# Kernel tuning notes

Measured on AMD Instinct MI355X. Metric: run time of the kernel, lower is better.

## Reference

```python
import jax, jax.numpy as jnp
import numpy as np

B, N, DIM, H, K = 2, 8192, 256, 8, 32
HD = DIM // H


def setup_inputs() -> dict:
    key = jax.random.key(0)
    ks = jax.random.split(key, 10)
    s = 1.0 / np.sqrt(DIM)
    return {
        "x": jax.random.normal(ks[0], (B, N, DIM), jnp.float32),
        "xyz": jax.random.normal(ks[1], (B, N, 3), jnp.float32),
        "idx": jax.random.randint(ks[2], (B, N, K), 0, N, jnp.int32),
        "Wq": jax.random.normal(ks[3], (DIM, DIM), jnp.float32) * s,
        "bq": jnp.zeros((DIM,), jnp.float32),
        "Wk": jax.random.normal(ks[4], (DIM, DIM), jnp.float32) * s,
        "bk": jnp.zeros((DIM,), jnp.float32),
        "Wv": jax.random.normal(ks[5], (DIM, DIM), jnp.float32) * s,
        "bv": jnp.zeros((DIM,), jnp.float32),
        "Wo": jax.random.normal(ks[6], (DIM, DIM), jnp.float32) * s,
        "bo": jnp.zeros((DIM,), jnp.float32),
        "W1": jax.random.normal(ks[7], (3, 32), jnp.float32) * 0.5,
        "b1": jnp.zeros((32,), jnp.float32),
        "W2": jax.random.normal(ks[8], (32, H), jnp.float32) * 0.2,
        "b2": jnp.zeros((H,), jnp.float32),
    }


def reference(x, xyz, idx, Wq, bq, Wk, bk, Wv, bv, Wo, bo, W1, b1, W2, b2):
    Bn, Nn, C = x.shape
    k = idx.shape[-1]
    q = (x @ Wq + bq).reshape(Bn, Nn, H, HD)          # [B,N,H,hd]
    kf = (x @ Wk + bk).reshape(Bn, Nn, H, HD)
    vf = (x @ Wv + bv).reshape(Bn, Nn, H, HD)
    # gather k neighbors per point (per-batch fancy indexing)
    gather = jax.vmap(lambda f, i: f[i])               # [N,H,hd],[N,k] -> [N,k,H,hd]
    kn = gather(kf, idx)                               # [B,N,k,H,hd]
    vn = gather(vf, idx)
    nxyz = jax.vmap(lambda p, i: p[i])(xyz, idx)       # [B,N,k,3]
    rel = xyz[:, :, None, :] - nxyz                    # [B,N,k,3]
    bias = jax.nn.relu(rel @ W1 + b1) @ W2 + b2        # [B,N,k,H]
    scores = jnp.einsum('bnhd,bnkhd->bnhk', q, kn) / np.sqrt(HD).astype(np.float32)
    scores = scores + bias.transpose(0, 1, 3, 2)       # [B,N,H,k]
    attn = jax.nn.softmax(scores, axis=-1)
    out = jnp.einsum('bnhk,bnkhd->bnhd', attn, vn).reshape(Bn, Nn, C)
    return out @ Wo + bo
```

## Files before the change

### kernel.cpp

```cpp
#include <hip/hip_runtime.h>
#include <hip/hip_bf16.h>

typedef unsigned int uint32;
typedef unsigned short ushort;
typedef __attribute__((ext_vector_type(4))) float floatx4;
typedef __attribute__((ext_vector_type(8))) __bf16 bf16x8;

#define NPTS 8192

__device__ __forceinline__ ushort f2bf(float f) {
    uint32 u = __float_as_uint(f);
    uint32 r = (u + 0x7fffu + ((u >> 16) & 1u)) >> 16;
    return (ushort)r;
}
__device__ __forceinline__ float bf1(ushort u) { return __uint_as_float((uint32)u << 16); }
__device__ __forceinline__ float bflo(uint32 u) { return __uint_as_float(u << 16); }
__device__ __forceinline__ float bfhi(uint32 u) { return __uint_as_float(u & 0xffff0000u); }

__global__ __launch_bounds__(256) void prep_kernel(
    const float* __restrict__ x, const float* __restrict__ xyz, const int* __restrict__ idx,
    const float* __restrict__ Wq, const float* __restrict__ Wk,
    const float* __restrict__ Wv, const float* __restrict__ Wo,
    const float* __restrict__ bq, const float* __restrict__ bk, const float* __restrict__ bv,
    const float* __restrict__ W1, const float* __restrict__ b1,
    const float* __restrict__ W2, const float* __restrict__ b2,
    ushort* __restrict__ xb, ushort* __restrict__ Wqkvt, ushort* __restrict__ Wot,
    float* __restrict__ biasqkv, ushort* __restrict__ bias_g) {
    const int bi = blockIdx.x;
    const int tid = threadIdx.x;
    if (bi < 4096) {
        int i = (bi * 256 + tid) * 4;
        float4 v = *(const float4*)(x + i);
        ushort4 o;
        o.x = f2bf(v.x); o.y = f2bf(v.y); o.z = f2bf(v.z); o.w = f2bf(v.w);
        *(ushort4*)(xb + i) = o;
    } else if (bi < 5120) {
        int f = (bi - 4096) * 256 + tid;
        if (f < 768 * 256) {
            int n = f >> 8, k = f & 255;
            int seg = n >> 8, nc = n & 255;
            const float* W = (seg == 0) ? Wq : (seg == 1) ? Wk : Wv;
            Wqkvt[f] = f2bf(W[k * 256 + nc]);
        } else {
            int g = f - 768 * 256;
            int n = g >> 8, k = g & 255;
            Wot[g] = f2bf(Wo[k * 256 + n]);
        }
        if (f < 768) biasqkv[f] = (f < 256) ? bq[f] : (f < 512) ? bk[f - 256] : bv[f - 512];
    } else {
        __shared__ float W1s[96], b1s[32], W2s[256], b2s[8];
        if (tid < 96) W1s[tid] = W1[tid];
        if (tid < 32) b1s[tid] = b1[tid];
        W2s[tid] = W2[tid];
        if (tid < 8) b2s[tid] = b2[tid];
        __syncthreads();
        const int wid = tid >> 6, lane = tid & 63;
        const int s = lane >> 5, j = lane & 31;
        const int p = (bi - 5120) * 8 + wid * 2 + s;
        const int b = p >> 13, n = p & 8191;
        const int nj = idx[(size_t)p * 32 + j];
        const size_t pb = ((size_t)b * NPTS + n) * 3;
        const size_t nb = ((size_t)b * NPTS + nj) * 3;
        const float rx = xyz[pb + 0] - xyz[nb + 0];
        const float ry = xyz[pb + 1] - xyz[nb + 1];
        const float rz = xyz[pb + 2] - xyz[nb + 2];
        float acc[8];
#pragma unroll
        for (int h = 0; h < 8; ++h) acc[h] = b2s[h];
#pragma unroll
        for (int u = 0; u < 32; ++u) {
            float hv = rx * W1s[u] + ry * W1s[32 + u] + rz * W1s[64 + u] + b1s[u];
            hv = fmaxf(hv, 0.f);
#pragma unroll
            for (int h = 0; h < 8; ++h) acc[h] += hv * W2s[u * 8 + h];
        }
#pragma unroll
        for (int h = 0; h < 8; ++h) bias_g[((size_t)p * 8 + h) * 32 + j] = f2bf(acc[h]);
    }
}

template <bool OUT_BF16>
__global__ __launch_bounds__(256) void gemm_mfma64(const ushort* __restrict__ A,
                                                   const ushort* __restrict__ Wt,
                                                   const float* __restrict__ bias,
                                                   void* __restrict__ outv, int N) {
    __shared__ __align__(16) ushort As[64 * 32];
    __shared__ __align__(16) ushort Bs[64 * 32];
    const int tid = threadIdx.x;
    const int w = tid >> 6, lane = tid & 63;
    const int m0 = blockIdx.y * 64, n0 = blockIdx.x * 64;

    const int row = tid >> 2;
    const int col16 = (tid & 3) * 16;

    floatx4 acc[4] = {};

    for (int kt = 0; kt < 256; kt += 32) {
        __syncthreads();
        {
            const char* ga = (const char*)(A + (size_t)(m0 + row) * 256 + kt) + col16;
            const char* gb = (const char*)(Wt + (size_t)(n0 + row) * 256 + kt) + col16;
            __builtin_amdgcn_global_load_lds((const __attribute__((address_space(1))) void*)ga,
                                             (__attribute__((address_space(3))) void*)((char*)As + w * 1024),
                                             16, 0, 0);
            __builtin_amdgcn_global_load_lds((const __attribute__((address_space(1))) void*)gb,
                                             (__attribute__((address_space(3))) void*)((char*)Bs + w * 1024),
                                             16, 0, 0);
        }
        __syncthreads();

        bf16x8 af = *(const bf16x8*)&As[(w * 16 + (lane & 15)) * 32 + (lane >> 4) * 8];
        bf16x8 bg[4];
#pragma unroll
        for (int ni = 0; ni < 4; ++ni)
            bg[ni] = *(const bf16x8*)&Bs[(ni * 16 + (lane & 15)) * 32 + (lane >> 4) * 8];
#pragma unroll
        for (int ni = 0; ni < 4; ++ni)
            acc[ni] = __builtin_amdgcn_mfma_f32_16x16x32_bf16(af, bg[ni], acc[ni], 0, 0, 0);
    }

#pragma unroll
    for (int ni = 0; ni < 4; ++ni) {
        const int col = n0 + ni * 16 + (lane & 15);
        const float bv = bias[col];
        const int row0 = m0 + w * 16 + (lane >> 4) * 4;
#pragma unroll
        for (int r = 0; r < 4; ++r) {
            const float v = acc[ni][r] + bv;
            if (OUT_BF16)
                ((ushort*)outv)[(size_t)(row0 + r) * N + col] = f2bf(v);
            else
                ((float*)outv)[(size_t)(row0 + r) * N + col] = v;
        }
    }
}

__global__ __launch_bounds__(256) void attn_kernel(
    const ushort* __restrict__ qkv, const int* __restrict__ idx,
    const ushort* __restrict__ bias_g, ushort* __restrict__ out) {
    __shared__ __align__(16) float q_s[4][2][32];
    __shared__ float e_s[4][2][32];
    __shared__ uint32 off_s[4][2][32];
    __shared__ float ssum_s[4][2];

    const int tid = threadIdx.x, wid = tid >> 6, lane = tid & 63;
    const int h = blockIdx.x & 7;
    const int pg = blockIdx.x >> 3;
    const int pbase = pg * 8 + wid * 2;
    const char* base = (const char*)qkv;

    const int s = lane >> 5, j = lane & 31;
    const int p = pbase + s;
    const int b = p >> 13;

    off_s[wid][s][j] = (uint32)(idx[(size_t)p * 32 + j] + b * NPTS) * 1536u;
    q_s[wid][s][j] = bf1(qkv[(size_t)p * 768 + h * 32 + j]);
    __syncthreads();

    {
        const uint4* kp = (const uint4*)(base + off_s[wid][s][j] + 512 + h * 64);
        float d = 0.f;
#pragma unroll
        for (int c = 0; c < 4; ++c) {
            uint4 kv = kp[c];
            float4 qa = *(const float4*)&q_s[wid][s][c * 8];
            float4 qb = *(const float4*)&q_s[wid][s][c * 8 + 4];
            d += bflo(kv.x) * qa.x + bfhi(kv.x) * qa.y
               + bflo(kv.y) * qa.z + bfhi(kv.y) * qa.w
               + bflo(kv.z) * qb.x + bfhi(kv.z) * qb.y
               + bflo(kv.w) * qb.z + bfhi(kv.w) * qb.w;
        }
        const float sc = d * 0.17677669529663687f + bf1(bias_g[((size_t)p * 8 + h) * 32 + j]);
        const float e = __expf(sc);
        float ssum = e;
#pragma unroll
        for (int msk = 16; msk >= 1; msk >>= 1) ssum += __shfl_xor(ssum, msk, 64);
        e_s[wid][s][j] = e;
        if (j == 0) ssum_s[wid][s] = ssum;
    }
    __syncthreads();

    {
        const int s2 = lane >> 5, hj = (lane >> 4) & 1, d2 = lane & 15;
        const int p2 = pbase + s2;
        const float rinv = __builtin_amdgcn_rcpf(ssum_s[wid][s2]);
        float ax = 0.f, ay = 0.f;
#pragma unroll
        for (int jj = 0; jj < 16; ++jj) {
            const int j2 = hj * 16 + jj;
            const float wgt = e_s[wid][s2][j2];
            const uint32 v = *(const uint32*)(base + off_s[wid][s2][j2] + 1024 + h * 64 + d2 * 4);
            ax += wgt * bflo(v);
            ay += wgt * bfhi(v);
        }
        ax += __shfl_xor(ax, 16, 64);
        ay += __shfl_xor(ay, 16, 64);
        if (hj == 0) {
            const uint32 o = (uint32)f2bf(ax * rinv) | ((uint32)f2bf(ay * rinv) << 16);
            *(uint32*)(out + (size_t)p2 * 256 + h * 32 + d2 * 2) = o;
        }
    }
}

extern "C" void kernel_launch(void* const* d_in, const int* in_sizes, int n_in,
                              void* d_out, int out_size, void* d_ws, size_t ws_size,
                              hipStream_t stream) {
    const float* x   = (const float*)d_in[0];
    const float* xyz = (const float*)d_in[1];
    const int*   idx = (const int*)d_in[2];
    const float* Wq = (const float*)d_in[3];
    const float* bq = (const float*)d_in[4];
    const float* Wk = (const float*)d_in[5];
    const float* bk = (const float*)d_in[6];
    const float* Wv = (const float*)d_in[7];
    const float* bv = (const float*)d_in[8];
    const float* Wo = (const float*)d_in[9];
    const float* bo = (const float*)d_in[10];
    const float* W1 = (const float*)d_in[11];
    const float* b1 = (const float*)d_in[12];
    const float* W2 = (const float*)d_in[13];
    const float* b2 = (const float*)d_in[14];

    char* wsb = (char*)d_ws;
    ushort* x_bf    = (ushort*)wsb;
    ushort* aout_bf = x_bf;
    ushort* qkv_bf  = (ushort*)(wsb + 8388608);
    ushort* Wqkvt   = (ushort*)(wsb + 33554432);
    ushort* Wot     = (ushort*)(wsb + 33947648);
    float*  biasqkv = (float*)(wsb + 34078720);
    ushort* bias_g  = (ushort*)(wsb + 34081792);

    prep_kernel<<<7168, 256, 0, stream>>>(x, xyz, idx, Wq, Wk, Wv, Wo, bq, bk, bv,
                                          W1, b1, W2, b2, x_bf, Wqkvt, Wot, biasqkv, bias_g);

    gemm_mfma64<true><<<dim3(12, 256), 256, 0, stream>>>(x_bf, Wqkvt, biasqkv, qkv_bf, 768);

    attn_kernel<<<16384, 256, 0, stream>>>(qkv_bf, idx, bias_g, aout_bf);

    gemm_mfma64<false><<<dim3(4, 256), 256, 0, stream>>>(aout_bf, Wot, bo, d_out, 256);
}
```

Before: 198.7 us.

## Use 128x128 swizzled-LDS tiles for QKV GEMM and vectorize attention V gather

```diff
diff --git a/kernel.cpp b/kernel.cpp
--- a/kernel.cpp
+++ b/kernel.cpp
@@ -79,17 +79,81 @@
     }
 }
 
-template <bool OUT_BF16>
+__global__ __launch_bounds__(256) void gemm_qkv(const ushort* __restrict__ A,
+                                                const ushort* __restrict__ Wt,
+                                                const float* __restrict__ bias,
+                                                ushort* __restrict__ outp) {
+    __shared__ __align__(16) ushort As[128 * 64];
+    __shared__ __align__(16) ushort Bs[128 * 64];
+    const int tid = threadIdx.x;
+    const int w = tid >> 6, lane = tid & 63;
+    const int m0 = blockIdx.y * 128, n0 = blockIdx.x * 128;
+    const int wm = (w & 1) * 64, wn = (w >> 1) * 64;
+    const int N = 768;
+
+    floatx4 acc[4][4] = {};
+
+    for (int kt = 0; kt < 256; kt += 64) {
+        __syncthreads();
+#pragma unroll
+        for (int c4 = 0; c4 < 4; ++c4) {
+            const int c = w * 4 + c4;
+            const int r = c * 8 + (lane >> 3);
+            const int gseg = (lane & 7) ^ (r & 7);
+            const char* ga = (const char*)(A + (size_t)(m0 + r) * 256 + kt) + gseg * 16;
+            const char* gb = (const char*)(Wt + (size_t)(n0 + r) * 256 + kt) + gseg * 16;
+            __builtin_amdgcn_global_load_lds((const __attribute__((address_space(1))) void*)ga,
+                                             (__attribute__((address_space(3))) void*)((char*)As + c * 1024),
+                                             16, 0, 0);
+            __builtin_amdgcn_global_load_lds((const __attribute__((address_space(1))) void*)gb,
+                                             (__attribute__((address_space(3))) void*)((char*)Bs + c * 1024),
+                                             16, 0, 0);
+        }
+        __syncthreads();
+
+        bf16x8 af[2][4], bg[2][4];
+#pragma unroll
+        for (int kk = 0; kk < 2; ++kk) {
+            const int s = kk * 4 + (lane >> 4);
+            const int phys = s ^ (lane & 7);
+#pragma unroll
+            for (int i = 0; i < 4; ++i) {
+                af[kk][i] = *(const bf16x8*)((const char*)As + (wm + i * 16 + (lane & 15)) * 128 + phys * 16);
+                bg[kk][i] = *(const bf16x8*)((const char*)Bs + (wn + i * 16 + (lane & 15)) * 128 + phys * 16);
+            }
+        }
+#pragma unroll
+        for (int kk = 0; kk < 2; ++kk)
+#pragma unroll
+            for (int mi = 0; mi < 4; ++mi)
+#pragma unroll
+                for (int ni = 0; ni < 4; ++ni)
+                    acc[mi][ni] = __builtin_amdgcn_mfma_f32_16x16x32_bf16(af[kk][mi], bg[kk][ni], acc[mi][ni], 0, 0, 0);
+    }
+
+#pragma unroll
+    for (int ni = 0; ni < 4; ++ni) {
+        const int col = n0 + wn + ni * 16 + (lane & 15);
+        const float bv = bias[col];
+#pragma unroll
+        for (int mi = 0; mi < 4; ++mi) {
+            const int row0 = m0 + wm + mi * 16 + (lane >> 4) * 4;
+#pragma unroll
+            for (int r = 0; r < 4; ++r)
+                outp[(size_t)(row0 + r) * N + col] = f2bf(acc[mi][ni][r] + bv);
+        }
+    }
+}
+
 __global__ __launch_bounds__(256) void gemm_mfma64(const ushort* __restrict__ A,
                                                    const ushort* __restrict__ Wt,
                                                    const float* __restrict__ bias,
-                                                   void* __restrict__ outv, int N) {
+                                                   float* __restrict__ outv, int N) {
     __shared__ __align__(16) ushort As[64 * 32];
     __shared__ __align__(16) ushort Bs[64 * 32];
     const int tid = threadIdx.x;
     const int w = tid >> 6, lane = tid & 63;
     const int m0 = blockIdx.y * 64, n0 = blockIdx.x * 64;
-
     const int row = tid >> 2;
     const int col16 = (tid & 3) * 16;
 
@@ -125,13 +189,8 @@
         const float bv = bias[col];
         const int row0 = m0 + w * 16 + (lane >> 4) * 4;
 #pragma unroll
-        for (int r = 0; r < 4; ++r) {
-            const float v = acc[ni][r] + bv;
-            if (OUT_BF16)
-                ((ushort*)outv)[(size_t)(row0 + r) * N + col] = f2bf(v);
-            else
-                ((float*)outv)[(size_t)(row0 + r) * N + col] = v;
-        }
+        for (int r = 0; r < 4; ++r)
+            outv[(size_t)(row0 + r) * N + col] = acc[ni][r] + bv;
     }
 }
 
@@ -181,23 +240,34 @@
     __syncthreads();
 
     {
-        const int s2 = lane >> 5, hj = (lane >> 4) & 1, d2 = lane & 15;
+        const int s2 = lane >> 5;
+        const int q4 = (lane >> 3) & 3;
+        const int j3 = lane & 7;
         const int p2 = pbase + s2;
-        const float rinv = __builtin_amdgcn_rcpf(ssum_s[wid][s2]);
-        float ax = 0.f, ay = 0.f;
-#pragma unroll
-        for (int jj = 0; jj < 16; ++jj) {
-            const int j2 = hj * 16 + jj;
+        float a[8] = {};
+#pragma unroll
+        for (int t = 0; t < 4; ++t) {
+            const int j2 = t * 8 + j3;
             const float wgt = e_s[wid][s2][j2];
-            const uint32 v = *(const uint32*)(base + off_s[wid][s2][j2] + 1024 + h * 64 + d2 * 4);
-            ax += wgt * bflo(v);
-            ay += wgt * bfhi(v);
-        }
-        ax += __shfl_xor(ax, 16, 64);
-        ay += __shfl_xor(ay, 16, 64);
-        if (hj == 0) {
-            const uint32 o = (uint32)f2bf(ax * rinv) | ((uint32)f2bf(ay * rinv) << 16);
-            *(uint32*)(out + (size_t)p2 * 256 + h * 32 + d2 * 2) = o;
+            const uint4 v = *(const uint4*)(base + off_s[wid][s2][j2] + 1024 + h * 64 + q4 * 16);
+            a[0] += wgt * bflo(v.x); a[1] += wgt * bfhi(v.x);
+            a[2] += wgt * bflo(v.y); a[3] += wgt * bfhi(v.y);
+            a[4] += wgt * bflo(v.z); a[5] += wgt * bfhi(v.z);
+            a[6] += wgt * bflo(v.w); a[7] += wgt * bfhi(v.w);
+        }
+#pragma unroll
+        for (int msk = 1; msk <= 4; msk <<= 1) {
+#pragma unroll
+            for (int d = 0; d < 8; ++d) a[d] += __shfl_xor(a[d], msk, 64);
+        }
+        if (j3 == 0) {
+            const float rinv = __builtin_amdgcn_rcpf(ssum_s[wid][s2]);
+            uint4 ov;
+            ov.x = (uint32)f2bf(a[0] * rinv) | ((uint32)f2bf(a[1] * rinv) << 16);
+            ov.y = (uint32)f2bf(a[2] * rinv) | ((uint32)f2bf(a[3] * rinv) << 16);
+            ov.z = (uint32)f2bf(a[4] * rinv) | ((uint32)f2bf(a[5] * rinv) << 16);
+            ov.w = (uint32)f2bf(a[6] * rinv) | ((uint32)f2bf(a[7] * rinv) << 16);
+            *(uint4*)(out + (size_t)p2 * 256 + h * 32 + q4 * 8) = ov;
         }
     }
 }
@@ -233,9 +303,9 @@
     prep_kernel<<<7168, 256, 0, stream>>>(x, xyz, idx, Wq, Wk, Wv, Wo, bq, bk, bv,
                                           W1, b1, W2, b2, x_bf, Wqkvt, Wot, biasqkv, bias_g);
 
-    gemm_mfma64<true><<<dim3(12, 256), 256, 0, stream>>>(x_bf, Wqkvt, biasqkv, qkv_bf, 768);
+    gemm_qkv<<<dim3(6, 128), 256, 0, stream>>>(x_bf, Wqkvt, biasqkv, qkv_bf);
 
     attn_kernel<<<16384, 256, 0, stream>>>(qkv_bf, idx, bias_g, aout_bf);
 
-    gemm_mfma64<false><<<dim3(4, 256), 256, 0, stream>>>(aout_bf, Wot, bo, d_out, 256);
-}
+    gemm_mfma64<<<dim3(4, 256), 256, 0, stream>>>(aout_bf, Wot, bo, (float*)d_out, 256);
+}
```

Result: no change. 198.4 us (-0.1%).
